# Kernel optimization log

Hardware: AMD Instinct MI355X
Metric: run time of the kernel (lower is better)

## Reference

```python
import jax, jax.numpy as jnp
import numpy as np

N_NODES = 100000
N_EDGES = 1600000
N_GRAPHS = 1000
F_IN, HID = 9, 64


def _glorot(key, shape):
    fan_in, fan_out = shape[0], shape[1]
    lim = (6.0 / (fan_in + fan_out)) ** 0.5
    return jax.random.uniform(key, shape, jnp.float32, -lim, lim)


def setup_inputs() -> dict:
    key = jax.random.key(0)
    ks = jax.random.split(key, 12)
    x = jax.random.normal(ks[0], (N_NODES, F_IN), jnp.float32)
    edge_index = jax.random.randint(ks[1], (2, N_EDGES), 0, N_NODES, jnp.int64)
    edge_attr = jnp.zeros((N_EDGES, 1), jnp.float32)
    batch = jnp.sort(jax.random.randint(ks[2], (N_NODES,), 0, N_GRAPHS, jnp.int64))
    # SAGEConv layer 1: 9 -> 64 (lin_l on aggregated neighbors w/ bias, lin_r on root)
    Wl1 = _glorot(ks[3], (F_IN, HID)); Wr1 = _glorot(ks[4], (F_IN, HID)); b1 = jnp.zeros((HID,), jnp.float32)
    # SAGEConv layer 2: 64 -> 64
    Wl2 = _glorot(ks[5], (HID, HID)); Wr2 = _glorot(ks[6], (HID, HID)); b2 = jnp.zeros((HID,), jnp.float32)
    # MLP readout: 64 -> 32 -> 1
    Wm1 = _glorot(ks[7], (HID, HID // 2)); bm1 = jnp.zeros((HID // 2,), jnp.float32)
    Wm2 = _glorot(ks[8], (HID // 2, 1)); bm2 = jnp.zeros((1,), jnp.float32)
    return dict(x=x, edge_index=edge_index, edge_attr=edge_attr, batch=batch,
                Wl1=Wl1, Wr1=Wr1, b1=b1, Wl2=Wl2, Wr2=Wr2, b2=b2,
                Wm1=Wm1, bm1=bm1, Wm2=Wm2, bm2=bm2)


def _sage_conv(x, src, dst, Wl, Wr, b, n_nodes):
    # mean aggregation of source-node features onto target nodes
    msgs = x[src]                                              # [E, F] gather
    s = jax.ops.segment_sum(msgs, dst, num_segments=n_nodes)   # [N, F] scatter-add
    cnt = jax.ops.segment_sum(jnp.ones((src.shape[0],), x.dtype), dst, num_segments=n_nodes)
    agg = s / jnp.maximum(cnt, 1.0)[:, None]
    return agg @ Wl + x @ Wr + b


def reference(x, edge_index, edge_attr, batch,
              Wl1, Wr1, b1, Wl2, Wr2, b2, Wm1, bm1, Wm2, bm2):
    src, dst = edge_index[0], edge_index[1]
    n = x.shape[0]
    h = jax.nn.relu(_sage_conv(x, src, dst, Wl1, Wr1, b1, n))
    h = _sage_conv(h, src, dst, Wl2, Wr2, b2, n)               # no act after last layer
    # global mean pool over graphs
    gs = jax.ops.segment_sum(h, batch, num_segments=N_GRAPHS)
    gc = jax.ops.segment_sum(jnp.ones((n,), h.dtype), batch, num_segments=N_GRAPHS)
    xg = gs / jnp.maximum(gc, 1.0)[:, None]                    # [G, 64]
    out = jax.nn.sigmoid(jax.nn.relu(xg @ Wm1 + bm1) @ Wm2 + bm2)  # [G, 1]
    return out
```

## Files before the change

### kernel.cpp

```cpp
#include <hip/hip_runtime.h>
#include <math.h>

#define N_NODES  100000
#define N_EDGES  1600000
#define N_GRAPHS 1000
#define F_IN     9
#define HID      64
#define NBUCK    196
#define BCAP     12288
#define CHUNK    4096
#define NZERO    128200

typedef unsigned int uint32;
typedef float v2f __attribute__((ext_vector_type(2)));


__device__ __forceinline__ uint32 pk_lo(float a, float b, uint32 old) {
    return (uint32)__builtin_amdgcn_cvt_pk_fp8_f32(a, b, (int)old, false);
}
__device__ __forceinline__ uint32 pk_hi(float a, float b, uint32 old) {
    return (uint32)__builtin_amdgcn_cvt_pk_fp8_f32(a, b, (int)old, true);
}

__global__ __launch_bounds__(256) void zero_kernel(float4* __restrict__ ws) {
    int i = blockIdx.x * 256 + threadIdx.x;
    if (i * 4 < NZERO)
        ws[i] = make_float4(0.f, 0.f, 0.f, 0.f);
}

__global__ __launch_bounds__(256) void pad_part_kernel(const float* __restrict__ x,
                                                       const int* __restrict__ ei,
                                                       int* __restrict__ gcur,
                                                       int* __restrict__ ebuf,
                                                       uint32* __restrict__ x8b) {
    __shared__ int lcnt[NBUCK], lbase[NBUCK];
    int tid = threadIdx.x;

    int n = blockIdx.x * 256 + tid;
    if (n < N_NODES) {
        uint32 w[4];
        #pragma unroll
        for (int p = 0; p < 4; ++p) {
            float v0 = (4 * p + 0 < F_IN) ? x[(size_t)n * F_IN + 4 * p + 0] : 0.0f;
            float v1 = (4 * p + 1 < F_IN) ? x[(size_t)n * F_IN + 4 * p + 1] : 0.0f;
            float v2 = (4 * p + 2 < F_IN) ? x[(size_t)n * F_IN + 4 * p + 2] : 0.0f;
            float v3 = (4 * p + 3 < F_IN) ? x[(size_t)n * F_IN + 4 * p + 3] : 0.0f;
            w[p] = pk_hi(v2, v3, pk_lo(v0, v1, 0u));
        }
        *reinterpret_cast<uint4*>(&x8b[(size_t)n * 4]) =
            make_uint4(w[0], w[1], w[2], w[3]);
    }

    for (int i = tid; i < NBUCK; i += 256) lcnt[i] = 0;
    __syncthreads();
    int e0 = blockIdx.x * CHUNK;
    int e1 = e0 + CHUNK; if (e1 > N_EDGES) e1 = N_EDGES;
    for (int e = e0 + tid; e < e1; e += 256)
        atomicAdd(&lcnt[ei[N_EDGES + e] >> 9], 1);
    __syncthreads();
    for (int i = tid; i < NBUCK; i += 256)
        lbase[i] = atomicAdd(&gcur[i], lcnt[i]);
    __syncthreads();
    for (int i = tid; i < NBUCK; i += 256) lcnt[i] = 0;
    __syncthreads();
    for (int e = e0 + tid; e < e1; e += 256) {
        int src = ei[e];
        int dst = ei[N_EDGES + e];
        int b = dst >> 9;
        int pos = lbase[b] + atomicAdd(&lcnt[b], 1);
        if (pos < BCAP)
            ebuf[(size_t)b * BCAP + pos] = src | ((dst & 511) << 17);
    }
}

__global__ __launch_bounds__(512) void build_csr_kernel(const int* __restrict__ ebuf,
                                                        const int* __restrict__ gcur,
                                                        int2* __restrict__ rowcnt,
                                                        int* __restrict__ col) {
    __shared__ int cnt[512];
    __shared__ int cur[512];
    __shared__ int wsum[8];
    int b = blockIdx.x;
    int n0 = b << 9;
    int tid = threadIdx.x;
    int ec = gcur[b]; if (ec > BCAP) ec = BCAP;
    size_t base = (size_t)b * BCAP;
    cnt[tid] = 0;
    __syncthreads();
    for (int e = tid; e < ec; e += 512)
        atomicAdd(&cnt[(uint32)ebuf[base + e] >> 17], 1);
    __syncthreads();
    int v = cnt[tid];
    int lane = tid & 63, wid = tid >> 6;
    int s = v;
    #pragma unroll
    for (int off = 1; off < 64; off <<= 1) {
        int u = __shfl_up(s, off, 64);
        if (lane >= off) s += u;
    }
    if (lane == 63) wsum[wid] = s;
    __syncthreads();
    int add = 0;
    for (int w = 0; w < wid; ++w) add += wsum[w];
    int off_ex = s - v + add;
    int n = n0 + tid;
    if (n < N_NODES) rowcnt[n] = make_int2((int)base + off_ex, v);
    cur[tid] = off_ex;
    __syncthreads();
    for (int e = tid; e < ec; e += 512) {
        int pv = ebuf[base + e];
        int pos = atomicAdd(&cur[(uint32)pv >> 17], 1);
        col[base + pos] = pv & 0x1FFFF;
    }
}

__global__ __launch_bounds__(256) void agg_l1_kernel(const float* __restrict__ x,
                                                     const uint32* __restrict__ x8b,
                                                     const int2* __restrict__ rowcnt,
                                                     const int* __restrict__ col,
                                                     const float* __restrict__ Wl1,
                                                     const float* __restrict__ Wr1,
                                                     const float* __restrict__ b1,
                                                     const int* __restrict__ batch,
                                                     uint32* __restrict__ h1b,
                                                     float* __restrict__ poolH) {
    __shared__ float w1s[F_IN * 128];
    __shared__ float bs[HID];
    __shared__ float ss[64 * 17];
    __shared__ float xs[64 * 10];
    __shared__ float hs[64 * 65];
    int tid = threadIdx.x;
    int n0 = blockIdx.x * 64;
    for (int i = tid; i < F_IN * HID; i += 256) {
        int f = i >> 6, j = i & 63;
        w1s[f * 128 + j]      = Wl1[i];
        w1s[f * 128 + 64 + j] = Wr1[i];
    }
    if (tid < HID) bs[tid] = b1[tid];
    for (int i = tid; i < 64 * F_IN; i += 256) {
        int r = i / F_IN, f = i - r * F_IN;
        int n = n0 + r;
        xs[r * 10 + f] = (n < N_NODES) ? x[(size_t)n * F_IN + f] : 0.0f;
    }

    {
        int r = tid >> 2, q = tid & 3;
        int n = n0 + r;
        v2f a01 = {0.f, 0.f}, a23 = {0.f, 0.f};
        int deg = 0;
        if (n < N_NODES) {
            int2 rc = rowcnt[n];
            deg = rc.y;
            int i = 0;
            for (; i + 1 < deg; i += 2) {
                int c0 = col[rc.x + i];
                int c1 = col[rc.x + i + 1];
                uint32 d0 = x8b[(size_t)c0 * 4 + q];
                uint32 d1 = x8b[(size_t)c1 * 4 + q];
                a01 += __builtin_amdgcn_cvt_pk_f32_fp8((int)d0, false);
                a23 += __builtin_amdgcn_cvt_pk_f32_fp8((int)d0, true);
                a01 += __builtin_amdgcn_cvt_pk_f32_fp8((int)d1, false);
                a23 += __builtin_amdgcn_cvt_pk_f32_fp8((int)d1, true);
            }
            if (i < deg) {
                uint32 d0 = x8b[(size_t)col[rc.x + i] * 4 + q];
                a01 += __builtin_amdgcn_cvt_pk_f32_fp8((int)d0, false);
                a23 += __builtin_amdgcn_cvt_pk_f32_fp8((int)d0, true);
            }
        }
        float inv = 1.0f / fmaxf((float)deg, 1.0f);
        int q4 = q * 4;
        ss[r * 17 + q4 + 0] = a01[0] * inv;
        ss[r * 17 + q4 + 1] = a01[1] * inv;
        ss[r * 17 + q4 + 2] = a23[0] * inv;
        ss[r * 17 + q4 + 3] = a23[1] * inv;
    }
    __syncthreads();

    int r = tid >> 2, cg = tid & 3, k0 = cg * 16;
    float h[16];
    #pragma unroll
    for (int kk = 0; kk < 16; ++kk) {
        int k = k0 + kk;
        float v = bs[k];
        #pragma unroll
        for (int f = 0; f < F_IN; ++f)
            v += ss[r * 17 + f] * w1s[f * 128 + k]
               + xs[r * 10 + f] * w1s[f * 128 + 64 + k];
        v = fmaxf(v, 0.0f);
        h[kk] = v;
        hs[r * 65 + k] = v;
    }
    int n = n0 + r;
    if (n < N_NODES) {
        uint32 w[4];
        #pragma unroll
        for (int p = 0; p < 4; ++p)
            w[p] = pk_hi(h[4 * p + 2], h[4 * p + 3],
                         pk_lo(h[4 * p + 0], h[4 * p + 1], 0u));
        *reinterpret_cast<uint4*>(&h1b[(size_t)n * 16 + cg * 4]) =
            make_uint4(w[0], w[1], w[2], w[3]);
    }
    __syncthreads();
    if (tid < HID) {
        int j = tid;
        int cur = batch[(n0 < N_NODES) ? n0 : (N_NODES - 1)];
        float v = (n0 < N_NODES) ? hs[0 * 65 + j] : 0.0f;
        for (int rr = 1; rr < 64; ++rr) {
            int nn = n0 + rr;
            bool ok = (nn < N_NODES);
            int g = batch[ok ? nn : (N_NODES - 1)];
            float val = ok ? hs[rr * 65 + j] : 0.0f;
            if (g == cur) v += val;
            else { atomicAdd(&poolH[cur * HID + j], v); cur = g; v = val; }
        }
        atomicAdd(&poolH[cur * HID + j], v);
    }
}

__global__ __launch_bounds__(256) void gather2_kernel(const uint32* __restrict__ h1b,
                                                      const int2* __restrict__ rowcnt,
                                                      const int* __restrict__ col,
                                                      const int* __restrict__ batch,
                                                      float* __restrict__ poolA) {
    __shared__ float sh[4][HID];
    int w = threadIdx.x >> 6;
    int lane = threadIdx.x & 63;
    int slot = lane >> 3;
    int grp  = lane & 7;
    int n = blockIdx.x * 4 + w;
    int2 rc = rowcnt[n];
    const uint32* hb = h1b + grp * 2;
    v2f a0 = {0.f, 0.f}, a1 = {0.f, 0.f}, a2 = {0.f, 0.f}, a3 = {0.f, 0.f};
    int i = rc.x + slot;
    int end = rc.x + rc.y;
    for (; i + 8 < end; i += 16) {
        int c0 = col[i];
        int c1 = col[i + 8];
        uint2 d0 = *reinterpret_cast<const uint2*>(hb + (size_t)c0 * 16);
        uint2 d1 = *reinterpret_cast<const uint2*>(hb + (size_t)c1 * 16);
        a0 += __builtin_amdgcn_cvt_pk_f32_fp8((int)d0.x, false);
        a1 += __builtin_amdgcn_cvt_pk_f32_fp8((int)d0.x, true);
        a2 += __builtin_amdgcn_cvt_pk_f32_fp8((int)d0.y, false);
        a3 += __builtin_amdgcn_cvt_pk_f32_fp8((int)d0.y, true);
        a0 += __builtin_amdgcn_cvt_pk_f32_fp8((int)d1.x, false);
        a1 += __builtin_amdgcn_cvt_pk_f32_fp8((int)d1.x, true);
        a2 += __builtin_amdgcn_cvt_pk_f32_fp8((int)d1.y, false);
        a3 += __builtin_amdgcn_cvt_pk_f32_fp8((int)d1.y, true);
    }
    if (i < end) {
        int c0 = col[i];
        uint2 d0 = *reinterpret_cast<const uint2*>(hb + (size_t)c0 * 16);
        a0 += __builtin_amdgcn_cvt_pk_f32_fp8((int)d0.x, false);
        a1 += __builtin_amdgcn_cvt_pk_f32_fp8((int)d0.x, true);
        a2 += __builtin_amdgcn_cvt_pk_f32_fp8((int)d0.y, false);
        a3 += __builtin_amdgcn_cvt_pk_f32_fp8((int)d0.y, true);
    }
    float r8[8] = {a0[0], a0[1], a1[0], a1[1], a2[0], a2[1], a3[0], a3[1]};
    #pragma unroll
    for (int k = 0; k < 8; ++k) {
        r8[k] += __shfl_xor(r8[k], 8, 64);
        r8[k] += __shfl_xor(r8[k], 16, 64);
        r8[k] += __shfl_xor(r8[k], 32, 64);
    }
    float inv = 1.0f / fmaxf((float)rc.y, 1.0f);
    if (slot == 0) {
        #pragma unroll
        for (int k = 0; k < 8; ++k)
            sh[w][grp * 8 + k] = r8[k] * inv;
    }
    __syncthreads();
    if (threadIdx.x < HID) {
        int j = threadIdx.x;
        int base = blockIdx.x * 4;
        int cur = batch[base];
        float v = sh[0][j];
        #pragma unroll
        for (int r = 1; r < 4; ++r) {
            int g = batch[base + r];
            float val = sh[r][j];
            if (g == cur) v += val;
            else { atomicAdd(&poolA[cur * HID + j], v); cur = g; v = val; }
        }
        atomicAdd(&poolA[cur * HID + j], v);
    }
}

__global__ void mlp_kernel(const float* __restrict__ poolA,
                           const float* __restrict__ poolH,
                           const int* __restrict__ batch,
                           const float* __restrict__ Wl2,
                           const float* __restrict__ Wr2,
                           const float* __restrict__ b2,
                           const float* __restrict__ Wm1,
                           const float* __restrict__ bm1,
                           const float* __restrict__ Wm2,
                           const float* __restrict__ bm2,
                           float* __restrict__ out) {
    __shared__ float spA[4][HID], spH[4][HID], sx[4][HID];
    int t = blockIdx.x * blockDim.x + threadIdx.x;
    int g = t >> 6;
    int j = t & 63;
    int w = threadIdx.x >> 6;
    if (g >= N_GRAPHS) return;
    int lo = 0, hi = N_NODES;
    while (lo < hi) { int m = (lo + hi) >> 1; if (batch[m] < g) lo = m + 1; else hi = m; }
    int start = lo;
    lo = 0; hi = N_NODES;
    while (lo < hi) { int m = (lo + hi) >> 1; if (batch[m] < g + 1) lo = m + 1; else hi = m; }
    int cntg = lo - start;
    float inv = 1.0f / fmaxf((float)cntg, 1.0f);
    spA[w][j] = poolA[g * HID + j];
    spH[w][j] = poolH[g * HID + j];
    float acc = 0.0f;
    #pragma unroll 8
    for (int k = 0; k < HID; ++k)
        acc += spA[w][k] * Wl2[k * HID + j] + spH[w][k] * Wr2[k * HID + j];
    sx[w][j] = acc * inv + b2[j];
    if (j < 32) {
        float a = bm1[j];
        #pragma unroll 8
        for (int k = 0; k < HID; ++k)
            a += sx[w][k] * Wm1[k * 32 + j];
        float r = fmaxf(a, 0.0f) * Wm2[j];
        #pragma unroll
        for (int off = 16; off > 0; off >>= 1)
            r += __shfl_down(r, off, 32);
        if (j == 0)
            out[g] = 1.0f / (1.0f + expf(-(r + bm2[0])));
    }
}

extern "C" void kernel_launch(void* const* d_in, const int* in_sizes, int n_in,
                              void* d_out, int out_size, void* d_ws, size_t ws_size,
                              hipStream_t stream) {
    const float* x    = (const float*)d_in[0];
    const int*   ei   = (const int*)d_in[1];
    const int*   batch= (const int*)d_in[3];
    const float* Wl1  = (const float*)d_in[4];
    const float* Wr1  = (const float*)d_in[5];
    const float* b1   = (const float*)d_in[6];
    const float* Wl2  = (const float*)d_in[7];
    const float* Wr2  = (const float*)d_in[8];
    const float* b2   = (const float*)d_in[9];
    const float* Wm1  = (const float*)d_in[10];
    const float* bm1  = (const float*)d_in[11];
    const float* Wm2  = (const float*)d_in[12];
    const float* bm2  = (const float*)d_in[13];
    float* out = (float*)d_out;

    int*   wsi = (int*)d_ws;
    float* wsf = (float*)d_ws;
    float*  poolA  = wsf;
    float*  poolH  = wsf + 64000;
    int*    gcur   = wsi + 128000;
    int2*   rowcnt = (int2*)(wsi + 128200);
    int*    col    = wsi + 328200;
    int*    ebuf   = wsi + 2736648;
    uint32* x8b    = (uint32*)(wsi + 5145096);
    uint32* h1b    = (uint32*)(wsi + 5545096);

    {
        int bl = (NZERO / 4 + 255) / 256;
        zero_kernel<<<bl, 256, 0, stream>>>((float4*)d_ws);
    }
    {   int bl = (N_EDGES + CHUNK - 1) / CHUNK;
        pad_part_kernel<<<bl, 256, 0, stream>>>(x, ei, gcur, ebuf, x8b);
    }
    build_csr_kernel<<<NBUCK, 512, 0, stream>>>(ebuf, gcur, rowcnt, col);
    {   int th = 256, bl = (N_NODES + 63) / 64;
        agg_l1_kernel<<<bl, th, 0, stream>>>(x, x8b, rowcnt, col, Wl1, Wr1, b1,
                                             batch, h1b, poolH);
    }
    {   int th = 256, bl = N_NODES / 4;
        gather2_kernel<<<bl, th, 0, stream>>>(h1b, rowcnt, col, batch, poolA);
    }
    {   int th = 256, bl = (N_GRAPHS * 64) / th;
        mlp_kernel<<<bl, th, 0, stream>>>(poolA, poolH, batch,
                                          Wl2, Wr2, b2, Wm1, bm1, Wm2, bm2, out);
    }
}
```

Before: 139.3 us.

## Split layer-1 neighbor aggregation across two lanes per node with 32 nodes per block

The layer-1 aggregation kernel now handles 32 nodes per block instead of 64. Each node's edge list is split between two lane groups (even and odd edges), each unrolled four deep, and the partial sums are combined with a shuffle. The projection stage gives each thread 8 output channels instead of 16, and the shared-memory staging of h for pooling is packed as bf16 pairs. Bounds checks are dropped because N_NODES divides evenly by 32. The aim is more memory-level parallelism and shorter serial degree loops, at the cost of twice as many blocks, twice as many pooling atomics and some bf16 rounding in the pooled sums.

```diff
diff --git a/kernel.cpp b/kernel.cpp
--- a/kernel.cpp
+++ b/kernel.cpp
@@ -10,8 +10,10 @@
 #define BCAP     12288
 #define CHUNK    4096
 #define NZERO    128200
+#define NPB      32
 
 typedef unsigned int uint32;
+typedef unsigned short ushort16;
 typedef float v2f __attribute__((ext_vector_type(2)));
 
 
@@ -20,6 +22,16 @@
 }
 __device__ __forceinline__ uint32 pk_hi(float a, float b, uint32 old) {
     return (uint32)__builtin_amdgcn_cvt_pk_fp8_f32(a, b, (int)old, true);
+}
+__device__ __forceinline__ float bfl(uint32 w) { return __uint_as_float(w << 16); }
+__device__ __forceinline__ float bfh(uint32 w) { return __uint_as_float(w & 0xffff0000u); }
+__device__ __forceinline__ uint32 f2bf1(float f) {
+    uint32 u = __float_as_uint(f);
+    u += 0x7fffu + ((u >> 16) & 1u);
+    return u >> 16;
+}
+__device__ __forceinline__ uint32 bfpair(float lo, float hi) {
+    return f2bf1(lo) | (f2bf1(hi) << 16);
 }
 
 __global__ __launch_bounds__(256) void zero_kernel(float4* __restrict__ ws) {
@@ -124,93 +136,102 @@
                                                      const int* __restrict__ batch,
                                                      uint32* __restrict__ h1b,
                                                      float* __restrict__ poolH) {
-    __shared__ float w1s[F_IN * 128];
-    __shared__ float bs[HID];
-    __shared__ float ss[64 * 17];
-    __shared__ float xs[64 * 10];
-    __shared__ float hs[64 * 65];
+    __shared__ float  w1s[F_IN * 128];
+    __shared__ float  bs[HID];
+    __shared__ float  ss[NPB * 20];
+    __shared__ float  xs[NPB * 10];
+    __shared__ uint32 hsp[NPB * 33];
     int tid = threadIdx.x;
-    int n0 = blockIdx.x * 64;
+    int n0 = blockIdx.x * NPB;
     for (int i = tid; i < F_IN * HID; i += 256) {
         int f = i >> 6, j = i & 63;
         w1s[f * 128 + j]      = Wl1[i];
         w1s[f * 128 + 64 + j] = Wr1[i];
     }
     if (tid < HID) bs[tid] = b1[tid];
-    for (int i = tid; i < 64 * F_IN; i += 256) {
+    for (int i = tid; i < NPB * F_IN; i += 256) {
         int r = i / F_IN, f = i - r * F_IN;
-        int n = n0 + r;
-        xs[r * 10 + f] = (n < N_NODES) ? x[(size_t)n * F_IN + f] : 0.0f;
+        xs[r * 10 + f] = x[(size_t)(n0 + r) * F_IN + f];
     }
 
     {
-        int r = tid >> 2, q = tid & 3;
-        int n = n0 + r;
+        int r = tid >> 3, s = (tid >> 2) & 1, q = tid & 3;
+        int2 rc = rowcnt[n0 + r];
+        int deg = rc.y;
         v2f a01 = {0.f, 0.f}, a23 = {0.f, 0.f};
-        int deg = 0;
-        if (n < N_NODES) {
-            int2 rc = rowcnt[n];
-            deg = rc.y;
-            int i = 0;
-            for (; i + 1 < deg; i += 2) {
-                int c0 = col[rc.x + i];
-                int c1 = col[rc.x + i + 1];
-                uint32 d0 = x8b[(size_t)c0 * 4 + q];
-                uint32 d1 = x8b[(size_t)c1 * 4 + q];
-                a01 += __builtin_amdgcn_cvt_pk_f32_fp8((int)d0, false);
-                a23 += __builtin_amdgcn_cvt_pk_f32_fp8((int)d0, true);
-                a01 += __builtin_amdgcn_cvt_pk_f32_fp8((int)d1, false);
-                a23 += __builtin_amdgcn_cvt_pk_f32_fp8((int)d1, true);
-            }
-            if (i < deg) {
-                uint32 d0 = x8b[(size_t)col[rc.x + i] * 4 + q];
-                a01 += __builtin_amdgcn_cvt_pk_f32_fp8((int)d0, false);
-                a23 += __builtin_amdgcn_cvt_pk_f32_fp8((int)d0, true);
-            }
-        }
-        float inv = 1.0f / fmaxf((float)deg, 1.0f);
-        int q4 = q * 4;
-        ss[r * 17 + q4 + 0] = a01[0] * inv;
-        ss[r * 17 + q4 + 1] = a01[1] * inv;
-        ss[r * 17 + q4 + 2] = a23[0] * inv;
-        ss[r * 17 + q4 + 3] = a23[1] * inv;
-    }
-    __syncthreads();
-
-    int r = tid >> 2, cg = tid & 3, k0 = cg * 16;
-    float h[16];
+        int i = s;
+        for (; i + 6 < deg; i += 8) {
+            int c0 = col[rc.x + i];
+            int c1 = col[rc.x + i + 2];
+            int c2 = col[rc.x + i + 4];
+            int c3 = col[rc.x + i + 6];
+            uint32 d0 = x8b[(size_t)c0 * 4 + q];
+            uint32 d1 = x8b[(size_t)c1 * 4 + q];
+            uint32 d2 = x8b[(size_t)c2 * 4 + q];
+            uint32 d3 = x8b[(size_t)c3 * 4 + q];
+            a01 += __builtin_amdgcn_cvt_pk_f32_fp8((int)d0, false);
+            a23 += __builtin_amdgcn_cvt_pk_f32_fp8((int)d0, true);
+            a01 += __builtin_amdgcn_cvt_pk_f32_fp8((int)d1, false);
+            a23 += __builtin_amdgcn_cvt_pk_f32_fp8((int)d1, true);
+            a01 += __builtin_amdgcn_cvt_pk_f32_fp8((int)d2, false);
+            a23 += __builtin_amdgcn_cvt_pk_f32_fp8((int)d2, true);
+            a01 += __builtin_amdgcn_cvt_pk_f32_fp8((int)d3, false);
+            a23 += __builtin_amdgcn_cvt_pk_f32_fp8((int)d3, true);
+        }
+        for (; i < deg; i += 2) {
+            uint32 d0 = x8b[(size_t)col[rc.x + i] * 4 + q];
+            a01 += __builtin_amdgcn_cvt_pk_f32_fp8((int)d0, false);
+            a23 += __builtin_amdgcn_cvt_pk_f32_fp8((int)d0, true);
+        }
+        float r4[4] = {a01[0], a01[1], a23[0], a23[1]};
+        #pragma unroll
+        for (int k = 0; k < 4; ++k)
+            r4[k] += __shfl_xor(r4[k], 4, 64);
+        if (s == 0) {
+            float inv = 1.0f / fmaxf((float)deg, 1.0f);
+            *reinterpret_cast<float4*>(&ss[r * 20 + q * 4]) =
+                make_float4(r4[0] * inv, r4[1] * inv, r4[2] * inv, r4[3] * inv);
+        }
+    }
+    __syncthreads();
+
+    int r = tid >> 3, cg = tid & 7, k0 = cg * 8;
+    float h[8];
     #pragma unroll
-    for (int kk = 0; kk < 16; ++kk) {
+    for (int kk = 0; kk < 8; ++kk) {
         int k = k0 + kk;
         float v = bs[k];
         #pragma unroll
         for (int f = 0; f < F_IN; ++f)
-            v += ss[r * 17 + f] * w1s[f * 128 + k]
+            v += ss[r * 20 + f] * w1s[f * 128 + k]
                + xs[r * 10 + f] * w1s[f * 128 + 64 + k];
-        v = fmaxf(v, 0.0f);
-        h[kk] = v;
-        hs[r * 65 + k] = v;
+        h[kk] = fmaxf(v, 0.0f);
     }
     int n = n0 + r;
-    if (n < N_NODES) {
-        uint32 w[4];
-        #pragma unroll
-        for (int p = 0; p < 4; ++p)
-            w[p] = pk_hi(h[4 * p + 2], h[4 * p + 3],
-                         pk_lo(h[4 * p + 0], h[4 * p + 1], 0u));
-        *reinterpret_cast<uint4*>(&h1b[(size_t)n * 16 + cg * 4]) =
-            make_uint4(w[0], w[1], w[2], w[3]);
+    {
+        uint32 w0 = pk_hi(h[2], h[3], pk_lo(h[0], h[1], 0u));
+        uint32 w1 = pk_hi(h[6], h[7], pk_lo(h[4], h[5], 0u));
+        *reinterpret_cast<uint2*>(&h1b[(size_t)n * 16 + cg * 2]) =
+            make_uint2(w0, w1);
+    }
+    {
+        hsp[r * 33 + cg * 4 + 0] = bfpair(h[0], h[1]);
+        hsp[r * 33 + cg * 4 + 1] = bfpair(h[2], h[3]);
+        hsp[r * 33 + cg * 4 + 2] = bfpair(h[4], h[5]);
+        hsp[r * 33 + cg * 4 + 3] = bfpair(h[6], h[7]);
     }
     __syncthreads();
     if (tid < HID) {
         int j = tid;
-        int cur = batch[(n0 < N_NODES) ? n0 : (N_NODES - 1)];
-        float v = (n0 < N_NODES) ? hs[0 * 65 + j] : 0.0f;
-        for (int rr = 1; rr < 64; ++rr) {
-            int nn = n0 + rr;
-            bool ok = (nn < N_NODES);
-            int g = batch[ok ? nn : (N_NODES - 1)];
-            float val = ok ? hs[rr * 65 + j] : 0.0f;
+        int wsel = j >> 1;
+        bool hi = (j & 1) != 0;
+        int cur = batch[n0];
+        uint32 w0 = hsp[wsel];
+        float v = hi ? bfh(w0) : bfl(w0);
+        for (int rr = 1; rr < NPB; ++rr) {
+            int g = batch[n0 + rr];
+            uint32 wr = hsp[rr * 33 + wsel];
+            float val = hi ? bfh(wr) : bfl(wr);
             if (g == cur) v += val;
             else { atomicAdd(&poolH[cur * HID + j], v); cur = g; v = val; }
         }
@@ -360,15 +381,14 @@
     uint32* x8b    = (uint32*)(wsi + 5145096);
     uint32* h1b    = (uint32*)(wsi + 5545096);
 
-    {
-        int bl = (NZERO / 4 + 255) / 256;
+    {   int bl = (NZERO / 4 + 255) / 256;
         zero_kernel<<<bl, 256, 0, stream>>>((float4*)d_ws);
     }
     {   int bl = (N_EDGES + CHUNK - 1) / CHUNK;
         pad_part_kernel<<<bl, 256, 0, stream>>>(x, ei, gcur, ebuf, x8b);
     }
     build_csr_kernel<<<NBUCK, 512, 0, stream>>>(ebuf, gcur, rowcnt, col);
-    {   int th = 256, bl = (N_NODES + 63) / 64;
+    {   int th = 256, bl = N_NODES / NPB;
         agg_l1_kernel<<<bl, th, 0, stream>>>(x, x8b, rowcnt, col, Wl1, Wr1, b1,
                                              batch, h1b, poolH);
     }
```

Result: faster. 130.2 us (-6.5%).
